# Kernel tuning notes

Measured on AMD Instinct MI355X. Metric: run time of the kernel, lower is better.

## Reference

```python
import jax, jax.numpy as jnp
import numpy as np

SPLIT = 3  # split_num: number of lead groups

def _hw_flatten(t, split):
    # [B,H,W,C] -> split along H into `split` groups, concat groups on channel axis,
    # then flatten spatial dims: result [B, (H/split)*W, split*C]
    B, H, W, C = t.shape
    hs = H // split
    t = t.reshape(B, split, hs, W, C).transpose(0, 2, 3, 1, 4)  # [B,hs,W,split,C]
    return t.reshape(B, hs * W, split * C)

def _hw_recover(o, B, hs, W, split, C):
    # inverse of _hw_flatten: [B, hs*W, split*C] -> [B, split*hs, W, C]
    o = o.reshape(B, hs, W, split, C).transpose(0, 3, 1, 2, 4)
    return o.reshape(B, split * hs, W, C)

def setup_inputs() -> dict:
    key = jax.random.key(0)
    kx, kf, kg, kh, kgam = jax.random.split(key, 5)
    B, H, W, C = 32, 12, 256, 256
    scale = 8
    Cf = C // scale
    x = jax.random.normal(kx, (B, H, W, C), dtype=jnp.float32)
    # 1x1 conv kernels == channel-mixing matrices [C_in, C_out], glorot-ish scale
    Wf = jax.random.normal(kf, (C, Cf), dtype=jnp.float32) * (2.0 / (C + Cf)) ** 0.5
    Wg = jax.random.normal(kg, (C, Cf), dtype=jnp.float32) * (2.0 / (C + Cf)) ** 0.5
    Wh = jax.random.normal(kh, (C, C), dtype=jnp.float32) * (1.0 / C) ** 0.5
    gamma = jax.random.normal(kgam, (1,), dtype=jnp.float32) * 0.1
    return {"x": x, "Wf": Wf, "Wg": Wg, "Wh": Wh, "gamma": gamma}

def reference(x, Wf, Wg, Wh, gamma):
    B, H, W, C = x.shape
    hs = H // SPLIT
    # 1x1 convs are per-pixel channel matmuls
    f = jnp.einsum('bhwc,cd->bhwd', x, Wf)
    g = jnp.einsum('bhwc,cd->bhwd', x, Wg)
    h = jnp.einsum('bhwc,cd->bhwd', x, Wh)
    f_fl = _hw_flatten(f, SPLIT)  # [B, N, SPLIT*Cf]
    g_fl = _hw_flatten(g, SPLIT)  # [B, N, SPLIT*Cf]
    h_fl = _hw_flatten(h, SPLIT)  # [B, N, SPLIT*C]
    # s = g @ f^T : [B, N, N]
    s = jnp.einsum('bnc,bmc->bnm', g_fl, f_fl)
    beta = jax.nn.softmax(s, axis=-1)
    o = jnp.einsum('bnm,bmc->bnc', beta, h_fl)  # [B, N, SPLIT*C]
    o = _hw_recover(o, B, hs, W, SPLIT, C)      # [B, H, W, C]
    return gamma * o + x
```

## Files before the change

### kernel.cpp

```cpp
#include <hip/hip_runtime.h>


typedef __bf16 bf16x8 __attribute__((ext_vector_type(8)));
typedef float f32x4 __attribute__((ext_vector_type(4)));

#define MFMA16 __builtin_amdgcn_mfma_f32_16x16x32_bf16

__device__ __forceinline__ short f2bf(float f) {
    unsigned u = __builtin_bit_cast(unsigned, f);
    u += 0x7fffu + ((u >> 16) & 1u);
    return (short)(u >> 16);
}
__device__ __forceinline__ unsigned pack2bf(float a, float b) {
    return ((unsigned)(unsigned short)f2bf(a)) |
           (((unsigned)(unsigned short)f2bf(b)) << 16);
}
__device__ __forceinline__ unsigned encf(float f) {
    unsigned u = __builtin_bit_cast(unsigned, f);
    return ((int)u < 0) ? ~u : (u | 0x80000000u);
}
__device__ __forceinline__ float decf(unsigned u) {
    unsigned v = (u & 0x80000000u) ? (u & 0x7fffffffu) : ~u;
    return __builtin_bit_cast(float, v);
}
__device__ __forceinline__ void gload_lds16(const short* g, short* l) {
    __builtin_amdgcn_global_load_lds(
        (const __attribute__((address_space(1))) unsigned int*)g,
        (__attribute__((address_space(3))) unsigned int*)l, 16, 0, 0);
}

__global__ __launch_bounds__(256) void wt_kernel(const float* __restrict__ Wf,
                                                 const float* __restrict__ Wg,
                                                 const float* __restrict__ Wh,
                                                 short* __restrict__ Wt,
                                                 unsigned* __restrict__ menc,
                                                 float* __restrict__ lsum) {
    int t = blockIdx.x * 256 + threadIdx.x;
    if (t < 32768) {
        menc[t] = 0u;
        lsum[t] = 0.f;
    }
    int j = t >> 8, k = t & 255;
    float v;
    if (j < 32)      v = Wf[k * 32 + j];
    else if (j < 64) v = Wg[k * 32 + (j - 32)];
    else             v = Wh[k * 256 + (j - 64)];
    Wt[j * 256 + k] = f2bf(v);
}

__global__ __launch_bounds__(256) void proj_kernel(const float* __restrict__ x,
                                                   const short* __restrict__ Wt,
                                                   short* __restrict__ f_fl,
                                                   short* __restrict__ g_fl,
                                                   short* __restrict__ h_t) {
    const int tid = threadIdx.x;
    const int P0  = blockIdx.x * 64;
    const int b   = P0 / 3072;
    const int rem = P0 % 3072;
    const int hh  = rem >> 8;
    const int wbase = rem & 255;
    const int lead = hh >> 2, hsi = hh & 3;
    const int nbase = hsi * 256 + wbase;

    __shared__ __align__(16) short smem[18432];
    __shared__ __align__(16) short sf[64 * 40];
    __shared__ __align__(16) short sg[64 * 40];
    short* xs = smem;

    const float4* xv = (const float4*)(x + (size_t)P0 * 256);
    #pragma unroll
    for (int i = 0; i < 16; ++i) {
        int idx = i * 256 + tid;
        float4 v = xv[idx];
        int pix = idx >> 6;
        int col = (idx & 63) * 4;
        *(short4*)&xs[pix * 264 + col] =
            make_short4(f2bf(v.x), f2bf(v.y), f2bf(v.z), f2bf(v.w));
    }
    __syncthreads();

    const int lane = tid & 63, wv = tid >> 6;
    const int quad = lane >> 4, l15 = lane & 15;

    {
        const int jrow = wv * 16 + l15;
        f32x4 acc[4] = {};
        #pragma unroll
        for (int ki = 0; ki < 8; ++ki) {
            bf16x8 a = *(const bf16x8*)&Wt[jrow * 256 + ki * 32 + quad * 8];
            #pragma unroll
            for (int pt = 0; pt < 4; ++pt) {
                bf16x8 bb = *(const bf16x8*)&xs[(pt * 16 + l15) * 264 + ki * 32 + quad * 8];
                acc[pt] = MFMA16(a, bb, acc[pt], 0, 0, 0);
            }
        }
        short* sdst = (wv < 2) ? sf : sg;
        const int jloc = (wv & 1) * 16 + quad * 4;
        #pragma unroll
        for (int pt = 0; pt < 4; ++pt)
            *(short4*)&sdst[(pt * 16 + l15) * 40 + jloc] =
                make_short4(f2bf(acc[pt][0]), f2bf(acc[pt][1]),
                            f2bf(acc[pt][2]), f2bf(acc[pt][3]));
    }

    f32x4 acc2[4][4] = {};
    #pragma unroll
    for (int ki = 0; ki < 8; ++ki) {
        bf16x8 a[4], bb[4];
        #pragma unroll
        for (int pt = 0; pt < 4; ++pt)
            a[pt] = *(const bf16x8*)&xs[(pt * 16 + l15) * 264 + ki * 32 + quad * 8];
        #pragma unroll
        for (int ct = 0; ct < 4; ++ct)
            bb[ct] = *(const bf16x8*)&Wt[(64 + wv * 64 + ct * 16 + l15) * 256 + ki * 32 + quad * 8];
        #pragma unroll
        for (int pt = 0; pt < 4; ++pt)
            #pragma unroll
            for (int ct = 0; ct < 4; ++ct)
                acc2[pt][ct] = MFMA16(a[pt], bb[ct], acc2[pt][ct], 0, 0, 0);
    }
    __syncthreads();

    short* sh = smem;
    #pragma unroll
    for (int pt = 0; pt < 4; ++pt)
        #pragma unroll
        for (int ct = 0; ct < 4; ++ct) {
            int cc = wv * 64 + ct * 16 + l15;
            *(short4*)&sh[cc * 72 + pt * 16 + quad * 4] =
                make_short4(f2bf(acc2[pt][ct][0]), f2bf(acc2[pt][ct][1]),
                            f2bf(acc2[pt][ct][2]), f2bf(acc2[pt][ct][3]));
        }

    {
        int r = tid >> 2, c = (tid & 3) * 8;
        size_t gbase = ((size_t)b * 1024 + nbase + r) * 96 + lead * 32 + c;
        *(int4*)&f_fl[gbase] = *(const int4*)&sf[r * 40 + c];
        *(int4*)&g_fl[gbase] = *(const int4*)&sg[r * 40 + c];
    }
    __syncthreads();

    #pragma unroll
    for (int p = 0; p < 8; ++p) {
        int row = p * 32 + (tid >> 3);
        int c   = (tid & 7) * 8;
        *(int4*)&h_t[((size_t)b * 768 + lead * 256 + row) * 1024 + nbase + c] =
            *(const int4*)&sh[row * 72 + c];
    }
}

__global__ __launch_bounds__(256) void smax_kernel(const short* __restrict__ f_fl,
                                                   const short* __restrict__ g_fl,
                                                   unsigned* __restrict__ menc) {
    const int qt = blockIdx.x, b = blockIdx.y;
    const int kt = qt;
    const int tid = threadIdx.x, lane = tid & 63, wv = tid >> 6;
    const int quad = lane >> 4, l15 = lane & 15;
    const int wm = (wv & 1) * 64, wn = (wv >> 1) * 64;
    const short* fB = f_fl + ((size_t)b * 1024 + kt * 128 + wm) * 96;
    const short* gB = g_fl + ((size_t)b * 1024 + qt * 128 + wn) * 96;

    bf16x8 bfr[4][3];
    #pragma unroll
    for (int j = 0; j < 4; ++j)
        #pragma unroll
        for (int ki = 0; ki < 3; ++ki)
            bfr[j][ki] = *(const bf16x8*)&gB[(j * 16 + l15) * 96 + ki * 32 + quad * 8];

    f32x4 acc[4][4] = {};
    #pragma unroll
    for (int i = 0; i < 4; ++i) {
        bf16x8 a[3];
        #pragma unroll
        for (int ki = 0; ki < 3; ++ki)
            a[ki] = *(const bf16x8*)&fB[(i * 16 + l15) * 96 + ki * 32 + quad * 8];
        #pragma unroll
        for (int j = 0; j < 4; ++j)
            #pragma unroll
            for (int ki = 0; ki < 3; ++ki)
                acc[i][j] = MFMA16(a[ki], bfr[j][ki], acc[i][j], 0, 0, 0);
    }

    #pragma unroll
    for (int j = 0; j < 4; ++j) {
        float v = acc[0][j][0];
        #pragma unroll
        for (int i = 0; i < 4; ++i)
            #pragma unroll
            for (int r = 0; r < 4; ++r) v = fmaxf(v, acc[i][j][r]);
        v = fmaxf(v, __shfl_xor(v, 16));
        v = fmaxf(v, __shfl_xor(v, 32));
        if (quad == 0)
            atomicMax(&menc[b * 1024 + qt * 128 + wn + j * 16 + l15], encf(v));
    }
}

__global__ __launch_bounds__(256) void pexp_kernel(const short* __restrict__ f_fl,
                                                   const short* __restrict__ g_fl,
                                                   const unsigned* __restrict__ menc,
                                                   float* __restrict__ lsum,
                                                   short* __restrict__ P) {
    const int kt = blockIdx.x, qt = blockIdx.y, b = blockIdx.z;
    const int tid = threadIdx.x, lane = tid & 63, wv = tid >> 6;
    const int quad = lane >> 4, l15 = lane & 15;
    const int wm = (wv & 1) * 64, wn = (wv >> 1) * 64;
    const short* fB = f_fl + ((size_t)b * 1024 + kt * 128 + wm) * 96;
    const short* gB = g_fl + ((size_t)b * 1024 + qt * 128 + wn) * 96;

    __shared__ __align__(16) short sP[128 * 136];

    bf16x8 bfr[4][3];
    #pragma unroll
    for (int j = 0; j < 4; ++j)
        #pragma unroll
        for (int ki = 0; ki < 3; ++ki)
            bfr[j][ki] = *(const bf16x8*)&gB[(j * 16 + l15) * 96 + ki * 32 + quad * 8];

    f32x4 acc[4][4] = {};
    #pragma unroll
    for (int i = 0; i < 4; ++i) {
        bf16x8 a[3];
        #pragma unroll
        for (int ki = 0; ki < 3; ++ki)
            a[ki] = *(const bf16x8*)&fB[(i * 16 + l15) * 96 + ki * 32 + quad * 8];
        #pragma unroll
        for (int j = 0; j < 4; ++j)
            #pragma unroll
            for (int ki = 0; ki < 3; ++ki)
                acc[i][j] = MFMA16(a[ki], bfr[j][ki], acc[i][j], 0, 0, 0);
    }

    #pragma unroll
    for (int j = 0; j < 4; ++j) {
        const int qloc = wn + j * 16 + l15;
        const float mj = decf(menc[b * 1024 + qt * 128 + qloc]);
        float rs = 0.f;
        #pragma unroll
        for (int i = 0; i < 4; ++i) {
            float e0 = __expf(acc[i][j][0] - mj);
            float e1 = __expf(acc[i][j][1] - mj);
            float e2 = __expf(acc[i][j][2] - mj);
            float e3 = __expf(acc[i][j][3] - mj);
            rs += (e0 + e1) + (e2 + e3);
            uint2 w;
            w.x = pack2bf(e0, e1);
            w.y = pack2bf(e2, e3);
            *(uint2*)&sP[qloc * 136 + wm + i * 16 + quad * 4] = w;
        }
        rs += __shfl_xor(rs, 16);
        rs += __shfl_xor(rs, 32);
        if (quad == 0)
            atomicAdd(&lsum[b * 1024 + qt * 128 + qloc], rs);
    }
    __syncthreads();

    short* Pb = (short*)P + (size_t)b * 1024 * 1024 + (size_t)(qt * 128) * 1024 + kt * 128;
    #pragma unroll
    for (int p = 0; p < 8; ++p) {
        int row = p * 16 + (tid >> 4);
        int c   = (tid & 15) * 8;
        *(int4*)&Pb[(size_t)row * 1024 + c] = *(const int4*)&sP[row * 136 + c];
    }
}

__global__ __launch_bounds__(256, 3) void gemm_kernel(const short* __restrict__ P,
                                                      const short* __restrict__ h_t,
                                                      const float* __restrict__ lsum,
                                                      const float* __restrict__ x,
                                                      const float* __restrict__ gammap,
                                                      float* __restrict__ out) {
    const int wgid = blockIdx.x;
    const int xcd  = wgid & 7;
    const int slot = wgid >> 3;
    const int b    = xcd * 4 + (slot / 48);
    const int t    = slot % 48;
    const int mt   = t % 6;
    const int nt   = t / 6;

    const int tid = threadIdx.x, lane = tid & 63, wv = tid >> 6;
    const int quad = lane >> 4, l15 = lane & 15;
    const int wm = (wv & 1) * 64, wn = (wv >> 1) * 64;

    __shared__ __align__(16) short As[3][128 * 32];
    __shared__ __align__(16) short Bs[3][128 * 32];

    const short* hB = h_t + ((size_t)b * 768 + mt * 128) * 1024;
    const short* Pb = P + ((size_t)b * 1024 + nt * 128) * 1024;

    const int srow  = wv * 16 + (lane >> 2);
    const int chunk = lane & 3;
    const int csw   = chunk ^ ((lane >> 3) & 3);
    const short* gA0 = hB + (size_t)srow * 1024 + csw * 8;
    const short* gA1 = hB + (size_t)(srow + 64) * 1024 + csw * 8;
    const short* gB0 = Pb + (size_t)srow * 1024 + csw * 8;
    const short* gB1 = Pb + (size_t)(srow + 64) * 1024 + csw * 8;
    const int ldst = srow * 32 + chunk * 8;

    const int ca = (quad ^ ((l15 >> 1) & 3)) * 8;

    f32x4 acc[4][4] = {};

#define STAGE_TILE(ktile, bufidx) do {                        \
        const int k0_ = (ktile) * 32;                         \
        short* a0_ = &As[bufidx][ldst];                       \
        short* b0_ = &Bs[bufidx][ldst];                       \
        gload_lds16(gA0 + k0_, a0_);                          \
        gload_lds16(gA1 + k0_, a0_ + 64 * 32);                \
        gload_lds16(gB0 + k0_, b0_);                          \
        gload_lds16(gB1 + k0_, b0_ + 64 * 32);                \
    } while (0)

    STAGE_TILE(0, 0);
    STAGE_TILE(1, 1);

    int cur = 0;
    for (int kt = 0; kt < 32; ++kt) {
        if (kt < 31) {
            asm volatile("s_waitcnt vmcnt(4)" ::: "memory");
        } else {
            asm volatile("s_waitcnt vmcnt(0)" ::: "memory");
        }
        __builtin_amdgcn_s_barrier();
        __builtin_amdgcn_sched_barrier(0);

        bf16x8 a[4], bb[4];
        #pragma unroll
        for (int i = 0; i < 4; ++i)
            a[i] = *(const bf16x8*)&As[cur][(wm + i * 16 + l15) * 32 + ca];
        #pragma unroll
        for (int j = 0; j < 4; ++j)
            bb[j] = *(const bf16x8*)&Bs[cur][(wn + j * 16 + l15) * 32 + ca];

        if (kt < 30) {
            const int nx = (cur == 0) ? 2 : cur - 1;
            STAGE_TILE(kt + 2, nx);
        }

        #pragma unroll
        for (int i = 0; i < 4; ++i)
            #pragma unroll
            for (int j = 0; j < 4; ++j)
                acc[i][j] = MFMA16(a[i], bb[j], acc[i][j], 0, 0, 0);

        cur = (cur == 2) ? 0 : cur + 1;
    }
#undef STAGE_TILE

    const float gamma = gammap[0];
    float gl[4];
    #pragma unroll
    for (int j = 0; j < 4; ++j)
        gl[j] = gamma / lsum[b * 1024 + nt * 128 + wn + j * 16 + l15];

    #pragma unroll
    for (int i = 0; i < 4; ++i)
        #pragma unroll
        for (int j = 0; j < 4; ++j) {
            int vc = mt * 128 + wm + i * 16 + quad * 4;
            int qrow = nt * 128 + wn + j * 16 + l15;
            int lead = vc >> 8, c = vc & 255;
            int hsi = qrow >> 8, w_ = qrow & 255;
            size_t idx = (((size_t)b * 12 + lead * 4 + hsi) * 256 + w_) * 256 + c;
            float4 xv = *(const float4*)&x[idx];
            float4 ov;
            ov.x = gl[j] * acc[i][j][0] + xv.x;
            ov.y = gl[j] * acc[i][j][1] + xv.y;
            ov.z = gl[j] * acc[i][j][2] + xv.z;
            ov.w = gl[j] * acc[i][j][3] + xv.w;
            *(float4*)&out[idx] = ov;
        }
}

extern "C" void kernel_launch(void* const* d_in, const int* in_sizes, int n_in,
                              void* d_out, int out_size, void* d_ws, size_t ws_size,
                              hipStream_t stream) {
    const float* x     = (const float*)d_in[0];
    const float* Wf    = (const float*)d_in[1];
    const float* Wg    = (const float*)d_in[2];
    const float* Wh    = (const float*)d_in[3];
    const float* gamma = (const float*)d_in[4];
    float* out = (float*)d_out;

    char* ws = (char*)d_ws;
    short*    Wt   = (short*)(ws + 0);
    short*    f_fl = (short*)(ws + 163840);
    short*    g_fl = (short*)(ws + 6455296);
    short*    h_t  = (short*)(ws + 12746752);
    short*    P    = (short*)(ws + 63078400);
    unsigned* menc = (unsigned*)(ws + 130187264);
    float*    lsum = (float*)(ws + 130318336);

    wt_kernel<<<dim3(320), dim3(256), 0, stream>>>(Wf, Wg, Wh, Wt, menc, lsum);
    proj_kernel<<<dim3(1536), dim3(256), 0, stream>>>(x, Wt, f_fl, g_fl, h_t);
    smax_kernel<<<dim3(8, 32), dim3(256), 0, stream>>>(f_fl, g_fl, menc);
    pexp_kernel<<<dim3(8, 8, 32), dim3(256), 0, stream>>>(f_fl, g_fl, menc, lsum, P);
    gemm_kernel<<<dim3(1536), dim3(256), 0, stream>>>(P, h_t, lsum, x, gamma, out);
}
```

Measured before the change: 326.8 us.

## Fuse softmax exponent and PV GEMM into one flash-style kernel

The separate max, exponent/P-materialization and PV GEMM kernels are replaced by one kernel. For each output tile it computes the row max from the diagonal key block, then loops over key blocks. Each iteration recomputes the QK^T scores, exponentiates them into LDS and multiplies them by h tiles loaded straight from global memory. Row sums are reduced in shared memory, so the 64MB bf16 P matrix and its global atomics are gone. The cost is recomputing the scores once per channel tile (6x) and giving up the LDS-staged, triple-buffered h/P pipeline of the old GEMM, with launch bounds changed to 2 waves.

New measurement: 626.8 us. +91.8%, slower.

```diff
diff --git a/kernel.cpp b/kernel.cpp
--- a/kernel.cpp
+++ b/kernel.cpp
@@ -15,31 +15,12 @@
     return ((unsigned)(unsigned short)f2bf(a)) |
            (((unsigned)(unsigned short)f2bf(b)) << 16);
 }
-__device__ __forceinline__ unsigned encf(float f) {
-    unsigned u = __builtin_bit_cast(unsigned, f);
-    return ((int)u < 0) ? ~u : (u | 0x80000000u);
-}
-__device__ __forceinline__ float decf(unsigned u) {
-    unsigned v = (u & 0x80000000u) ? (u & 0x7fffffffu) : ~u;
-    return __builtin_bit_cast(float, v);
-}
-__device__ __forceinline__ void gload_lds16(const short* g, short* l) {
-    __builtin_amdgcn_global_load_lds(
-        (const __attribute__((address_space(1))) unsigned int*)g,
-        (__attribute__((address_space(3))) unsigned int*)l, 16, 0, 0);
-}
 
 __global__ __launch_bounds__(256) void wt_kernel(const float* __restrict__ Wf,
                                                  const float* __restrict__ Wg,
                                                  const float* __restrict__ Wh,
-                                                 short* __restrict__ Wt,
-                                                 unsigned* __restrict__ menc,
-                                                 float* __restrict__ lsum) {
+                                                 short* __restrict__ Wt) {
     int t = blockIdx.x * 256 + threadIdx.x;
-    if (t < 32768) {
-        menc[t] = 0u;
-        lsum[t] = 0.f;
-    }
     int j = t >> 8, k = t & 255;
     float v;
     if (j < 32)      v = Wf[k * 32 + j];
@@ -149,208 +130,148 @@
     }
 }
 
-__global__ __launch_bounds__(256) void smax_kernel(const short* __restrict__ f_fl,
-                                                   const short* __restrict__ g_fl,
-                                                   unsigned* __restrict__ menc) {
-    const int qt = blockIdx.x, b = blockIdx.y;
-    const int kt = qt;
-    const int tid = threadIdx.x, lane = tid & 63, wv = tid >> 6;
-    const int quad = lane >> 4, l15 = lane & 15;
-    const int wm = (wv & 1) * 64, wn = (wv >> 1) * 64;
-    const short* fB = f_fl + ((size_t)b * 1024 + kt * 128 + wm) * 96;
-    const short* gB = g_fl + ((size_t)b * 1024 + qt * 128 + wn) * 96;
-
-    bf16x8 bfr[4][3];
-    #pragma unroll
-    for (int j = 0; j < 4; ++j)
-        #pragma unroll
-        for (int ki = 0; ki < 3; ++ki)
-            bfr[j][ki] = *(const bf16x8*)&gB[(j * 16 + l15) * 96 + ki * 32 + quad * 8];
-
-    f32x4 acc[4][4] = {};
-    #pragma unroll
-    for (int i = 0; i < 4; ++i) {
-        bf16x8 a[3];
-        #pragma unroll
-        for (int ki = 0; ki < 3; ++ki)
-            a[ki] = *(const bf16x8*)&fB[(i * 16 + l15) * 96 + ki * 32 + quad * 8];
-        #pragma unroll
-        for (int j = 0; j < 4; ++j)
-            #pragma unroll
-            for (int ki = 0; ki < 3; ++ki)
-                acc[i][j] = MFMA16(a[ki], bfr[j][ki], acc[i][j], 0, 0, 0);
-    }
-
-    #pragma unroll
-    for (int j = 0; j < 4; ++j) {
-        float v = acc[0][j][0];
-        #pragma unroll
-        for (int i = 0; i < 4; ++i)
-            #pragma unroll
-            for (int r = 0; r < 4; ++r) v = fmaxf(v, acc[i][j][r]);
-        v = fmaxf(v, __shfl_xor(v, 16));
-        v = fmaxf(v, __shfl_xor(v, 32));
-        if (quad == 0)
-            atomicMax(&menc[b * 1024 + qt * 128 + wn + j * 16 + l15], encf(v));
-    }
-}
-
-__global__ __launch_bounds__(256) void pexp_kernel(const short* __restrict__ f_fl,
-                                                   const short* __restrict__ g_fl,
-                                                   const unsigned* __restrict__ menc,
-                                                   float* __restrict__ lsum,
-                                                   short* __restrict__ P) {
-    const int kt = blockIdx.x, qt = blockIdx.y, b = blockIdx.z;
-    const int tid = threadIdx.x, lane = tid & 63, wv = tid >> 6;
-    const int quad = lane >> 4, l15 = lane & 15;
-    const int wm = (wv & 1) * 64, wn = (wv >> 1) * 64;
-    const short* fB = f_fl + ((size_t)b * 1024 + kt * 128 + wm) * 96;
-    const short* gB = g_fl + ((size_t)b * 1024 + qt * 128 + wn) * 96;
-
-    __shared__ __align__(16) short sP[128 * 136];
-
-    bf16x8 bfr[4][3];
-    #pragma unroll
-    for (int j = 0; j < 4; ++j)
-        #pragma unroll
-        for (int ki = 0; ki < 3; ++ki)
-            bfr[j][ki] = *(const bf16x8*)&gB[(j * 16 + l15) * 96 + ki * 32 + quad * 8];
-
-    f32x4 acc[4][4] = {};
-    #pragma unroll
-    for (int i = 0; i < 4; ++i) {
-        bf16x8 a[3];
-        #pragma unroll
-        for (int ki = 0; ki < 3; ++ki)
-            a[ki] = *(const bf16x8*)&fB[(i * 16 + l15) * 96 + ki * 32 + quad * 8];
-        #pragma unroll
-        for (int j = 0; j < 4; ++j)
-            #pragma unroll
-            for (int ki = 0; ki < 3; ++ki)
-                acc[i][j] = MFMA16(a[ki], bfr[j][ki], acc[i][j], 0, 0, 0);
-    }
-
-    #pragma unroll
-    for (int j = 0; j < 4; ++j) {
-        const int qloc = wn + j * 16 + l15;
-        const float mj = decf(menc[b * 1024 + qt * 128 + qloc]);
-        float rs = 0.f;
-        #pragma unroll
-        for (int i = 0; i < 4; ++i) {
-            float e0 = __expf(acc[i][j][0] - mj);
-            float e1 = __expf(acc[i][j][1] - mj);
-            float e2 = __expf(acc[i][j][2] - mj);
-            float e3 = __expf(acc[i][j][3] - mj);
-            rs += (e0 + e1) + (e2 + e3);
-            uint2 w;
-            w.x = pack2bf(e0, e1);
-            w.y = pack2bf(e2, e3);
-            *(uint2*)&sP[qloc * 136 + wm + i * 16 + quad * 4] = w;
-        }
-        rs += __shfl_xor(rs, 16);
-        rs += __shfl_xor(rs, 32);
-        if (quad == 0)
-            atomicAdd(&lsum[b * 1024 + qt * 128 + qloc], rs);
-    }
-    __syncthreads();
-
-    short* Pb = (short*)P + (size_t)b * 1024 * 1024 + (size_t)(qt * 128) * 1024 + kt * 128;
-    #pragma unroll
-    for (int p = 0; p < 8; ++p) {
-        int row = p * 16 + (tid >> 4);
-        int c   = (tid & 15) * 8;
-        *(int4*)&Pb[(size_t)row * 1024 + c] = *(const int4*)&sP[row * 136 + c];
-    }
-}
-
-__global__ __launch_bounds__(256, 3) void gemm_kernel(const short* __restrict__ P,
-                                                      const short* __restrict__ h_t,
-                                                      const float* __restrict__ lsum,
-                                                      const float* __restrict__ x,
-                                                      const float* __restrict__ gammap,
-                                                      float* __restrict__ out) {
+__global__ __launch_bounds__(256, 2) void fused_kernel(const short* __restrict__ f_fl,
+                                                       const short* __restrict__ g_fl,
+                                                       const short* __restrict__ h_t,
+                                                       const float* __restrict__ x,
+                                                       const float* __restrict__ gammap,
+                                                       float* __restrict__ out) {
     const int wgid = blockIdx.x;
     const int xcd  = wgid & 7;
     const int slot = wgid >> 3;
     const int b    = xcd * 4 + (slot / 48);
     const int t    = slot % 48;
-    const int mt   = t % 6;
-    const int nt   = t / 6;
+    const int mt   = t >> 3;
+    const int nt   = t & 7;
 
     const int tid = threadIdx.x, lane = tid & 63, wv = tid >> 6;
     const int quad = lane >> 4, l15 = lane & 15;
     const int wm = (wv & 1) * 64, wn = (wv >> 1) * 64;
-
-    __shared__ __align__(16) short As[3][128 * 32];
-    __shared__ __align__(16) short Bs[3][128 * 32];
-
-    const short* hB = h_t + ((size_t)b * 768 + mt * 128) * 1024;
-    const short* Pb = P + ((size_t)b * 1024 + nt * 128) * 1024;
-
-    const int srow  = wv * 16 + (lane >> 2);
-    const int chunk = lane & 3;
-    const int csw   = chunk ^ ((lane >> 3) & 3);
-    const short* gA0 = hB + (size_t)srow * 1024 + csw * 8;
-    const short* gA1 = hB + (size_t)(srow + 64) * 1024 + csw * 8;
-    const short* gB0 = Pb + (size_t)srow * 1024 + csw * 8;
-    const short* gB1 = Pb + (size_t)(srow + 64) * 1024 + csw * 8;
-    const int ldst = srow * 32 + chunk * 8;
-
-    const int ca = (quad ^ ((l15 >> 1) & 3)) * 8;
-
-    f32x4 acc[4][4] = {};
-
-#define STAGE_TILE(ktile, bufidx) do {                        \
-        const int k0_ = (ktile) * 32;                         \
-        short* a0_ = &As[bufidx][ldst];                       \
-        short* b0_ = &Bs[bufidx][ldst];                       \
-        gload_lds16(gA0 + k0_, a0_);                          \
-        gload_lds16(gA1 + k0_, a0_ + 64 * 32);                \
-        gload_lds16(gB0 + k0_, b0_);                          \
-        gload_lds16(gB1 + k0_, b0_ + 64 * 32);                \
-    } while (0)
-
-    STAGE_TILE(0, 0);
-    STAGE_TILE(1, 1);
-
-    int cur = 0;
-    for (int kt = 0; kt < 32; ++kt) {
-        if (kt < 31) {
-            asm volatile("s_waitcnt vmcnt(4)" ::: "memory");
-        } else {
-            asm volatile("s_waitcnt vmcnt(0)" ::: "memory");
-        }
-        __builtin_amdgcn_s_barrier();
-        __builtin_amdgcn_sched_barrier(0);
-
-        bf16x8 a[4], bb[4];
-        #pragma unroll
-        for (int i = 0; i < 4; ++i)
-            a[i] = *(const bf16x8*)&As[cur][(wm + i * 16 + l15) * 32 + ca];
-        #pragma unroll
-        for (int j = 0; j < 4; ++j)
-            bb[j] = *(const bf16x8*)&Bs[cur][(wn + j * 16 + l15) * 32 + ca];
-
-        if (kt < 30) {
-            const int nx = (cur == 0) ? 2 : cur - 1;
-            STAGE_TILE(kt + 2, nx);
-        }
-
-        #pragma unroll
-        for (int i = 0; i < 4; ++i)
+    const int half = wv & 1;
+
+    __shared__ __align__(16) short sP[128 * 136];
+    __shared__ float sM[2][128];
+    __shared__ float sL[2][128];
+
+    const short* gB    = g_fl + ((size_t)b * 1024 + nt * 128 + wn) * 96;
+    const short* fBase = f_fl + ((size_t)b * 1024 + wm) * 96;
+    const short* hB    = h_t  + ((size_t)b * 768 + mt * 128) * 1024;
+
+    bf16x8 bfr[4][3];
+    #pragma unroll
+    for (int j = 0; j < 4; ++j)
+        #pragma unroll
+        for (int ki = 0; ki < 3; ++ki)
+            bfr[j][ki] = *(const bf16x8*)&gB[(j * 16 + l15) * 96 + ki * 32 + quad * 8];
+
+    {
+        const short* fB = fBase + (size_t)(nt * 128) * 96;
+        f32x4 acc[4][4] = {};
+        #pragma unroll
+        for (int i = 0; i < 4; ++i) {
+            bf16x8 a[3];
+            #pragma unroll
+            for (int ki = 0; ki < 3; ++ki)
+                a[ki] = *(const bf16x8*)&fB[(i * 16 + l15) * 96 + ki * 32 + quad * 8];
             #pragma unroll
             for (int j = 0; j < 4; ++j)
-                acc[i][j] = MFMA16(a[i], bb[j], acc[i][j], 0, 0, 0);
-
-        cur = (cur == 2) ? 0 : cur + 1;
-    }
-#undef STAGE_TILE
+                #pragma unroll
+                for (int ki = 0; ki < 3; ++ki)
+                    acc[i][j] = MFMA16(a[ki], bfr[j][ki], acc[i][j], 0, 0, 0);
+        }
+        #pragma unroll
+        for (int j = 0; j < 4; ++j) {
+            float v = acc[0][j][0];
+            #pragma unroll
+            for (int i = 0; i < 4; ++i)
+                #pragma unroll
+                for (int r = 0; r < 4; ++r) v = fmaxf(v, acc[i][j][r]);
+            v = fmaxf(v, __shfl_xor(v, 16));
+            v = fmaxf(v, __shfl_xor(v, 32));
+            if (quad == 0) sM[half][wn + j * 16 + l15] = v;
+        }
+    }
+    __syncthreads();
+
+    float mj[4], rsum[4];
+    #pragma unroll
+    for (int j = 0; j < 4; ++j) {
+        int r = wn + j * 16 + l15;
+        mj[j] = fmaxf(sM[0][r], sM[1][r]);
+        rsum[j] = 0.f;
+    }
+
+    f32x4 accp[4][4] = {};
+
+    #pragma unroll 1
+    for (int g = 0; g < 8; ++g) {
+        const short* fB = fBase + (size_t)(g * 128) * 96;
+        f32x4 acc[4][4] = {};
+        #pragma unroll
+        for (int i = 0; i < 4; ++i) {
+            bf16x8 a[3];
+            #pragma unroll
+            for (int ki = 0; ki < 3; ++ki)
+                a[ki] = *(const bf16x8*)&fB[(i * 16 + l15) * 96 + ki * 32 + quad * 8];
+            #pragma unroll
+            for (int j = 0; j < 4; ++j)
+                #pragma unroll
+                for (int ki = 0; ki < 3; ++ki)
+                    acc[i][j] = MFMA16(a[ki], bfr[j][ki], acc[i][j], 0, 0, 0);
+        }
+        #pragma unroll 1
+        for (int j = 0; j < 4; ++j) {
+            const int qloc = wn + j * 16 + l15;
+            float rs = 0.f;
+            #pragma unroll
+            for (int i = 0; i < 4; ++i) {
+                float e0 = __expf(acc[i][j][0] - mj[j]);
+                float e1 = __expf(acc[i][j][1] - mj[j]);
+                float e2 = __expf(acc[i][j][2] - mj[j]);
+                float e3 = __expf(acc[i][j][3] - mj[j]);
+                rs += (e0 + e1) + (e2 + e3);
+                uint2 w;
+                w.x = pack2bf(e0, e1);
+                w.y = pack2bf(e2, e3);
+                *(uint2*)&sP[qloc * 136 + wm + i * 16 + quad * 4] = w;
+            }
+            rs += __shfl_xor(rs, 16);
+            rs += __shfl_xor(rs, 32);
+            rsum[j] += rs;
+        }
+        __syncthreads();
+
+        #pragma unroll
+        for (int kk = 0; kk < 4; ++kk) {
+            const int k0 = g * 128 + kk * 32;
+            bf16x8 ah[4], bb[4];
+            #pragma unroll
+            for (int i = 0; i < 4; ++i)
+                ah[i] = *(const bf16x8*)&hB[(size_t)(wm + i * 16 + l15) * 1024 + k0 + quad * 8];
+            #pragma unroll
+            for (int j = 0; j < 4; ++j)
+                bb[j] = *(const bf16x8*)&sP[(wn + j * 16 + l15) * 136 + kk * 32 + quad * 8];
+            #pragma unroll
+            for (int i = 0; i < 4; ++i)
+                #pragma unroll
+                for (int j = 0; j < 4; ++j)
+                    accp[i][j] = MFMA16(ah[i], bb[j], accp[i][j], 0, 0, 0);
+        }
+        __syncthreads();
+    }
+
+    #pragma unroll
+    for (int j = 0; j < 4; ++j)
+        if (quad == 0) sL[half][wn + j * 16 + l15] = rsum[j];
+    __syncthreads();
 
     const float gamma = gammap[0];
     float gl[4];
     #pragma unroll
-    for (int j = 0; j < 4; ++j)
-        gl[j] = gamma / lsum[b * 1024 + nt * 128 + wn + j * 16 + l15];
+    for (int j = 0; j < 4; ++j) {
+        int r = wn + j * 16 + l15;
+        gl[j] = gamma / (sL[0][r] + sL[1][r]);
+    }
 
     #pragma unroll
     for (int i = 0; i < 4; ++i)
@@ -363,10 +284,10 @@
             size_t idx = (((size_t)b * 12 + lead * 4 + hsi) * 256 + w_) * 256 + c;
             float4 xv = *(const float4*)&x[idx];
             float4 ov;
-            ov.x = gl[j] * acc[i][j][0] + xv.x;
-            ov.y = gl[j] * acc[i][j][1] + xv.y;
-            ov.z = gl[j] * acc[i][j][2] + xv.z;
-            ov.w = gl[j] * acc[i][j][3] + xv.w;
+            ov.x = gl[j] * accp[i][j][0] + xv.x;
+            ov.y = gl[j] * accp[i][j][1] + xv.y;
+            ov.z = gl[j] * accp[i][j][2] + xv.z;
+            ov.w = gl[j] * accp[i][j][3] + xv.w;
             *(float4*)&out[idx] = ov;
         }
 }
@@ -382,17 +303,12 @@
     float* out = (float*)d_out;
 
     char* ws = (char*)d_ws;
-    short*    Wt   = (short*)(ws + 0);
-    short*    f_fl = (short*)(ws + 163840);
-    short*    g_fl = (short*)(ws + 6455296);
-    short*    h_t  = (short*)(ws + 12746752);
-    short*    P    = (short*)(ws + 63078400);
-    unsigned* menc = (unsigned*)(ws + 130187264);
-    float*    lsum = (float*)(ws + 130318336);
-
-    wt_kernel<<<dim3(320), dim3(256), 0, stream>>>(Wf, Wg, Wh, Wt, menc, lsum);
+    short* Wt   = (short*)(ws + 0);
+    short* f_fl = (short*)(ws + 163840);
+    short* g_fl = (short*)(ws + 6455296);
+    short* h_t  = (short*)(ws + 12746752);
+
+    wt_kernel<<<dim3(320), dim3(256), 0, stream>>>(Wf, Wg, Wh, Wt);
     proj_kernel<<<dim3(1536), dim3(256), 0, stream>>>(x, Wt, f_fl, g_fl, h_t);
-    smax_kernel<<<dim3(8, 32), dim3(256), 0, stream>>>(f_fl, g_fl, menc);
-    pexp_kernel<<<dim3(8, 8, 32), dim3(256), 0, stream>>>(f_fl, g_fl, menc, lsum, P);
-    gemm_kernel<<<dim3(1536), dim3(256), 0, stream>>>(P, h_t, lsum, x, gamma, out);
-}
+    fused_kernel<<<dim3(1536), dim3(256), 0, stream>>>(f_fl, g_fl, h_t, x, gamma, out);
+}
```
